# Performance work log

Measured on AMD Instinct MI355X. Metric: run time of the kernel, lower is better.

Reference implementation:

```python
import jax, jax.numpy as jnp
import numpy as np
import math

D, NH, NL, NP_ = 256, 8, 3, 4
BS, LQ = 32, 300
SHAPES = [(80, 80), (40, 40), (20, 20)]
LV = sum(h * w for h, w in SHAPES)  # 8400
DFF = 1024


def _offset_bias():
    # faithful to MSDeformableAttention._reset_parameters
    thetas = jnp.arange(NH, dtype=jnp.float32) * (2.0 * math.pi / NH)
    grid = jnp.stack([jnp.cos(thetas), jnp.sin(thetas)], -1)
    grid = grid / jnp.abs(grid).max(-1, keepdims=True)
    grid = jnp.tile(grid.reshape(NH, 1, 1, 2), (1, NL, NP_, 1))
    grid = grid * jnp.arange(1, NP_ + 1, dtype=jnp.float32).reshape(1, 1, -1, 1)
    return grid.reshape(-1)


def setup_inputs() -> dict:
    key = jax.random.key(0)
    ks = iter(jax.random.split(key, 64))
    rn = lambda shape, s=0.02: jax.random.normal(next(ks), shape, jnp.float32) * s
    z = lambda n: jnp.zeros((n,), jnp.float32)
    o = lambda n: jnp.ones((n,), jnp.float32)
    inp = {
        'tgt': jax.random.normal(next(ks), (BS, LQ, D), jnp.float32),
        'reference_points': jax.random.uniform(next(ks), (BS, LQ, NL, 2), jnp.float32),
        'memory': jax.random.normal(next(ks), (BS, LV, D), jnp.float32),
        'query_pos_embed': jax.random.normal(next(ks), (BS, LQ, D), jnp.float32),
        'memory_spatial_shapes': np.array(SHAPES, dtype=np.int64),
        'memory_level_start_index': np.array([0, 6400, 8000], dtype=np.int64),
        # self-attn
        'Wq': rn((D, D)), 'bq': z(D), 'Wk': rn((D, D)), 'bk': z(D),
        'Wv': rn((D, D)), 'bv': z(D), 'Wo': rn((D, D)), 'bo': z(D),
        'ln1_g': o(D), 'ln1_b': z(D),
        # deformable cross-attn
        'W_vproj': rn((D, D)), 'b_vproj': z(D),
        'W_off': rn((D, NH * NL * NP_ * 2), 0.001), 'b_off': _offset_bias(),
        'W_attn': rn((D, NH * NL * NP_)), 'b_attn': z(NH * NL * NP_),
        'W_out': rn((D, D)), 'b_out': z(D),
        'ln2_g': o(D), 'ln2_b': z(D),
        # FFN
        'W1': rn((D, DFF)), 'b1': z(DFF), 'W2': rn((DFF, D)), 'b2': z(D),
        'ln3_g': o(D), 'ln3_b': z(D),
    }
    return inp


def _ln(x, g, b):
    m = x.mean(-1, keepdims=True)
    v = ((x - m) ** 2).mean(-1, keepdims=True)
    return (x - m) / jnp.sqrt(v + 1e-5) * g + b


def _ms_deform(value, shapes, loc, aw):
    # value [bs,Lv,nh,c]; loc [bs,Lq,nh,NL,NP,2] in [0,1]; aw [bs,Lq,nh,NL,NP]
    bs, Lv, nh, c = value.shape
    Lq = loc.shape[1]
    npts = loc.shape[4]
    grids = 2.0 * loc - 1.0
    out = jnp.zeros((bs, nh, Lq, c), value.dtype)
    start = 0
    for lvl, (h, w) in enumerate(shapes):
        flat = value[:, start:start + h * w].transpose(0, 2, 1, 3)  # [bs,nh,hw,c]
        start += h * w
        g = grids[:, :, :, lvl].transpose(0, 2, 1, 3, 4).reshape(bs, nh, Lq * npts, 2)
        # align_corners=False pixel coords
        x = (g[..., 0] + 1.0) * (w / 2.0) - 0.5
        y = (g[..., 1] + 1.0) * (h / 2.0) - 0.5
        x0 = jnp.floor(x); y0 = jnp.floor(y)
        wx1 = x - x0; wy1 = y - y0
        samp = jnp.zeros((bs, nh, Lq * npts, c), value.dtype)
        for xi, yi, wgt in ((x0, y0, (1 - wx1) * (1 - wy1)),
                            (x0 + 1, y0, wx1 * (1 - wy1)),
                            (x0, y0 + 1, (1 - wx1) * wy1),
                            (x0 + 1, y0 + 1, wx1 * wy1)):
            valid = (xi >= 0) & (xi < w) & (yi >= 0) & (yi < h)
            idx = (jnp.clip(yi, 0, h - 1) * w + jnp.clip(xi, 0, w - 1)).astype(jnp.int32)
            idx = jnp.broadcast_to(idx[..., None], idx.shape + (c,))
            gv = jnp.take_along_axis(flat, idx, axis=2)  # [bs,nh,Lq*np,c]
            samp = samp + gv * (wgt * valid.astype(value.dtype))[..., None]
        samp = samp.reshape(bs, nh, Lq, npts, c)
        a = aw[:, :, :, lvl].transpose(0, 2, 1, 3)  # [bs,nh,Lq,np]
        out = out + (samp * a[..., None]).sum(3)
    return out.transpose(0, 2, 1, 3).reshape(bs, Lq, nh * c)


def reference(tgt, reference_points, memory, query_pos_embed,
              memory_spatial_shapes, memory_level_start_index,
              Wq, bq, Wk, bk, Wv, bv, Wo, bo, ln1_g, ln1_b,
              W_vproj, b_vproj, W_off, b_off, W_attn, b_attn, W_out, b_out,
              ln2_g, ln2_b, W1, b1, W2, b2, ln3_g, ln3_b):
    shapes = [(int(h), int(w)) for h, w in np.asarray(memory_spatial_shapes)]
    bs, Lq, d = tgt.shape
    hd = d // NH
    # --- self attention (dropout=eval identity, attn_mask=None) ---
    q = tgt + query_pos_embed
    qh = (q @ Wq + bq).reshape(bs, Lq, NH, hd)
    kh = (q @ Wk + bk).reshape(bs, Lq, NH, hd)
    vh = (tgt @ Wv + bv).reshape(bs, Lq, NH, hd)
    att = jax.nn.softmax(jnp.einsum('bqhd,bkhd->bhqk', qh, kh) / jnp.sqrt(jnp.float32(hd)), axis=-1)
    sa = jnp.einsum('bhqk,bkhd->bqhd', att, vh).reshape(bs, Lq, d) @ Wo + bo
    tgt = _ln(tgt + sa, ln1_g, ln1_b)
    # --- deformable cross attention ---
    qc = tgt + query_pos_embed
    value = (memory @ W_vproj + b_vproj).reshape(bs, -1, NH, hd)
    off = (qc @ W_off + b_off).reshape(bs, Lq, NH, NL, NP_, 2)
    aw = jax.nn.softmax((qc @ W_attn + b_attn).reshape(bs, Lq, NH, NL * NP_), axis=-1)
    aw = aw.reshape(bs, Lq, NH, NL, NP_)
    norm = jnp.array([[w, h] for h, w in shapes], jnp.float32)  # flip -> (w,h)
    loc = reference_points[:, :, None, :, None, :] + off / norm[None, None, None, :, None, :]
    ca = _ms_deform(value, shapes, loc, aw) @ W_out + b_out
    tgt = _ln(tgt + ca, ln2_g, ln2_b)
    # --- FFN ---
    h = jax.nn.relu(tgt @ W1 + b1) @ W2 + b2
    return _ln(tgt + h, ln3_g, ln3_b)
```

## Files before the change

### kernel.cpp

```cpp
#include <hip/hip_runtime.h>
#include <hip/hip_bf16.h>

#define D_      256
#define NH_     8
#define HD_     32
#define NL_     3
#define NP_4    4
#define BS_     32
#define LQ_     300
#define LV_     8400
#define DFF_    1024
#define NTOK    (BS_ * LQ_)
#define NVAL    (BS_ * LV_)

typedef __attribute__((ext_vector_type(8))) short bf16x8;
typedef __attribute__((ext_vector_type(4))) float f32x4;

__device__ inline unsigned short f2bf(float x) {
    union { float f; unsigned u; } v; v.f = x;
    unsigned r = v.u + 0x7FFFu + ((v.u >> 16) & 1u);
    return (unsigned short)(r >> 16);
}
__device__ inline float bf2f(unsigned short x) {
    union { unsigned u; float f; } v; v.u = ((unsigned)x) << 16;
    return v.f;
}

struct TrDesc { const float* W; unsigned short* Wt; int K; int N; };
struct TrPack { TrDesc d[10]; };

__global__ __launch_bounds__(256)
void tr_kernel(TrPack p) {
    TrDesc d = p.d[blockIdx.z];
    const int n0 = blockIdx.x * 32, k0 = blockIdx.y * 32;
    if (n0 >= d.N || k0 >= d.K) return;
    __shared__ float t[32][33];
    const int tx = threadIdx.x & 31, ty = threadIdx.x >> 5;
    #pragma unroll
    for (int i = 0; i < 4; ++i) {
        int k = k0 + ty + i * 8, n = n0 + tx;
        t[ty + i * 8][tx] = (k < d.K && n < d.N) ? d.W[(size_t)k * d.N + n] : 0.f;
    }
    __syncthreads();
    #pragma unroll
    for (int i = 0; i < 4; ++i) {
        int n = n0 + ty + i * 8, k = k0 + tx;
        if (n < d.N && k < d.K) d.Wt[(size_t)n * d.K + k] = f2bf(t[tx][ty + i * 8]);
    }
}

template <int ROWS, int COLS, int KK, int KC, int WR, int WC, int AMODE, int CMODE>
__global__ __launch_bounds__(256)
void gemm_os(const void* __restrict__ Ain, const float* __restrict__ A2,
             const unsigned short* __restrict__ Wt, const float* __restrict__ bias,
             void* __restrict__ Cout, int M, int N) {
    constexpr int LDK = KC + 8;
    constexpr int NC = KK / KC;
    constexpr int KS = KC / 32;
    constexpr int WROWS = ROWS / WR, WCOLS = COLS / WC;
    constexpr int RT = WROWS / 16, TC = WCOLS / 16;
    __shared__ unsigned short Alds[ROWS * LDK];
    __shared__ unsigned short Blds[COLS * LDK];

    const int tid = threadIdx.x, lane = tid & 63, w = tid >> 6;
    const int quad = lane >> 4, l16 = lane & 15;
    const int wr = w / WC, wc = w % WC;
    const int rowBase = blockIdx.y * ROWS;
    const int colBase = blockIdx.x * COLS;

    f32x4 acc[RT][TC];
    #pragma unroll
    for (int rt = 0; rt < RT; ++rt)
        #pragma unroll
        for (int j = 0; j < TC; ++j)
            #pragma unroll
            for (int r = 0; r < 4; ++r) acc[rt][j][r] = 0.f;

    for (int ch = 0; ch < NC; ++ch) {
        if (NC > 1) __syncthreads();
        {
            constexpr int CNT = ROWS * KC / 1024;
            if (AMODE == 2) {
                constexpr int CNT2 = ROWS * KC / 2048;
                #pragma unroll
                for (int i = 0; i < CNT2; ++i) {
                    int idx = i * 256 + tid;
                    int row = idx / (KC / 8), kofs = (idx % (KC / 8)) * 8;
                    int4 v = *(const int4*)((const unsigned short*)Ain +
                              (size_t)(rowBase + row) * KK + ch * KC + kofs);
                    *(int4*)&Alds[row * LDK + kofs] = v;
                }
            } else {
                #pragma unroll
                for (int i = 0; i < CNT; ++i) {
                    int idx = i * 256 + tid;
                    int row = idx / (KC / 4), kofs = (idx % (KC / 4)) * 4;
                    size_t g = (size_t)(rowBase + row) * KK + ch * KC + kofs;
                    float4 a = *(const float4*)((const float*)Ain + g);
                    if (AMODE == 1) {
                        float4 b = *(const float4*)(A2 + g);
                        a.x += b.x; a.y += b.y; a.z += b.z; a.w += b.w;
                    }
                    ushort4 s4;
                    s4.x = f2bf(a.x); s4.y = f2bf(a.y);
                    s4.z = f2bf(a.z); s4.w = f2bf(a.w);
                    *(ushort4*)&Alds[row * LDK + kofs] = s4;
                }
            }
        }
        {
            constexpr int CNT = COLS * KC / 2048;
            #pragma unroll
            for (int i = 0; i < CNT; ++i) {
                int idx = i * 256 + tid;
                int col = idx / (KC / 8), kofs = (idx % (KC / 8)) * 8;
                int4 v = *(const int4*)(Wt + (size_t)(colBase + col) * KK + ch * KC + kofs);
                *(int4*)&Blds[col * LDK + kofs] = v;
            }
        }
        __syncthreads();

        #pragma unroll
        for (int s = 0; s < KS; ++s) {
            bf16x8 af[RT], bf[TC];
            #pragma unroll
            for (int rt = 0; rt < RT; ++rt)
                af[rt] = *(const bf16x8*)&Alds[(wr * WROWS + rt * 16 + l16) * LDK + s * 32 + quad * 8];
            #pragma unroll
            for (int j = 0; j < TC; ++j)
                bf[j] = *(const bf16x8*)&Blds[(wc * WCOLS + j * 16 + l16) * LDK + s * 32 + quad * 8];
            #pragma unroll
            for (int rt = 0; rt < RT; ++rt)
                #pragma unroll
                for (int j = 0; j < TC; ++j)
                    acc[rt][j] = __builtin_amdgcn_mfma_f32_16x16x32_bf16(af[rt], bf[j], acc[rt][j], 0, 0, 0);
        }
    }

    #pragma unroll
    for (int rt = 0; rt < RT; ++rt) {
        #pragma unroll
        for (int j = 0; j < TC; ++j) {
            int col = colBase + wc * WCOLS + j * 16 + l16;
            float bb = bias[col];
            #pragma unroll
            for (int r = 0; r < 4; ++r) {
                int row = rowBase + wr * WROWS + rt * 16 + quad * 4 + r;
                float c = acc[rt][j][r] + bb;
                if (CMODE == 1 || CMODE == 3) c = fmaxf(c, 0.f);
                if (CMODE >= 2)
                    ((unsigned short*)Cout)[(size_t)row * N + col] = f2bf(c);
                else
                    ((float*)Cout)[(size_t)row * N + col] = c;
            }
        }
    }
}

#define PS_STRIDE 344
__global__ __launch_bounds__(256)
void attn_mfma(const unsigned short* __restrict__ qh,
               const unsigned short* __restrict__ kh,
               const unsigned short* __restrict__ vh,
               float* __restrict__ out) {
    __shared__ unsigned short Ps[4 * 16 * PS_STRIDE];
    __shared__ unsigned short Vs[32 * PS_STRIDE];
    const int tid = threadIdx.x;
    const int bh = blockIdx.x >> 1, half_ = blockIdx.x & 1;
    const int b = bh >> 3, h = bh & 7;
    const int w = tid >> 6, lane = tid & 63;
    const int quad = lane >> 4, l16 = lane & 15;

    for (int i = tid; i < 4 * 16 * PS_STRIDE / 2; i += 256) ((unsigned*)Ps)[i] = 0u;

    const size_t hbase = ((size_t)b * LQ_) * D_ + h * HD_;
    for (int it = 0; it < 10; ++it) {
        int chunk = tid + 256 * it;
        int key = chunk >> 3, cc = (chunk & 7) * 4;
        ushort4 v = make_ushort4(0, 0, 0, 0);
        if (key < LQ_) v = *(const ushort4*)(vh + hbase + (size_t)key * D_ + cc);
        Vs[(cc + 0) * PS_STRIDE + key] = v.x;
        Vs[(cc + 1) * PS_STRIDE + key] = v.y;
        Vs[(cc + 2) * PS_STRIDE + key] = v.z;
        Vs[(cc + 3) * PS_STRIDE + key] = v.w;
    }
    __syncthreads();

    const unsigned short* qb = qh + hbase;
    const unsigned short* kb = kh + hbase;
    const float scale = 0.17677669529663687f;

    for (int qt = 10 * half_ + w; qt < 10 * half_ + 10 && qt < 19; qt += 4) {
        int rowq = qt * 16 + l16; if (rowq > LQ_ - 1) rowq = LQ_ - 1;
        bf16x8 aq = *(const bf16x8*)(qb + (size_t)rowq * D_ + quad * 8);

        f32x4 S[19];
        #pragma unroll
        for (int kt = 0; kt < 19; ++kt) {
            int rowk = kt * 16 + l16; if (rowk > LQ_ - 1) rowk = LQ_ - 1;
            bf16x8 bk = *(const bf16x8*)(kb + (size_t)rowk * D_ + quad * 8);
            f32x4 z; z[0] = z[1] = z[2] = z[3] = 0.f;
            S[kt] = __builtin_amdgcn_mfma_f32_16x16x32_bf16(aq, bk, z, 0, 0, 0);
        }
        float mrow[4] = {-1e30f, -1e30f, -1e30f, -1e30f};
        #pragma unroll
        for (int kt = 0; kt < 19; ++kt) {
            bool masked = (kt == 18) && (l16 >= 12);
            #pragma unroll
            for (int r = 0; r < 4; ++r) {
                float s = masked ? -1e30f : S[kt][r] * scale;
                S[kt][r] = s;
                mrow[r] = fmaxf(mrow[r], s);
            }
        }
        #pragma unroll
        for (int r = 0; r < 4; ++r)
            #pragma unroll
            for (int off = 1; off < 16; off <<= 1)
                mrow[r] = fmaxf(mrow[r], __shfl_xor(mrow[r], off));
        float psum[4] = {0.f, 0.f, 0.f, 0.f};
        #pragma unroll
        for (int kt = 0; kt < 19; ++kt)
            #pragma unroll
            for (int r = 0; r < 4; ++r) {
                float p = __expf(S[kt][r] - mrow[r]);
                S[kt][r] = p;
                psum[r] += p;
            }
        #pragma unroll
        for (int r = 0; r < 4; ++r)
            #pragma unroll
            for (int off = 1; off < 16; off <<= 1)
                psum[r] += __shfl_xor(psum[r], off);
        float linv[4];
        #pragma unroll
        for (int r = 0; r < 4; ++r) linv[r] = 1.f / psum[r];

        unsigned short* pw = Ps + w * (16 * PS_STRIDE);
        #pragma unroll
        for (int kt = 0; kt < 19; ++kt)
            #pragma unroll
            for (int r = 0; r < 4; ++r)
                pw[(quad * 4 + r) * PS_STRIDE + kt * 16 + l16] = f2bf(S[kt][r]);

        f32x4 o0, o1;
        #pragma unroll
        for (int r = 0; r < 4; ++r) { o0[r] = 0.f; o1[r] = 0.f; }
        #pragma unroll
        for (int ks = 0; ks < 10; ++ks) {
            bf16x8 ap = *(const bf16x8*)(pw + l16 * PS_STRIDE + ks * 32 + quad * 8);
            bf16x8 b0 = *(const bf16x8*)(Vs + l16 * PS_STRIDE + ks * 32 + quad * 8);
            bf16x8 b1 = *(const bf16x8*)(Vs + (16 + l16) * PS_STRIDE + ks * 32 + quad * 8);
            o0 = __builtin_amdgcn_mfma_f32_16x16x32_bf16(ap, b0, o0, 0, 0, 0);
            o1 = __builtin_amdgcn_mfma_f32_16x16x32_bf16(ap, b1, o1, 0, 0, 0);
        }
        #pragma unroll
        for (int r = 0; r < 4; ++r) {
            int q = qt * 16 + quad * 4 + r;
            if (q < LQ_) {
                size_t ob = ((size_t)b * LQ_ + q) * D_ + h * HD_;
                out[ob + l16]      = o0[r] * linv[r];
                out[ob + 16 + l16] = o1[r] * linv[r];
            }
        }
    }
}

__global__ __launch_bounds__(256)
void ln_kernel(const float* __restrict__ x, const float* __restrict__ r,
               const float* __restrict__ g, const float* __restrict__ bta,
               float* __restrict__ out) {
    const int tok = blockIdx.x;
    const int t = threadIdx.x;
    float v = x[(size_t)tok * D_ + t] + r[(size_t)tok * D_ + t];

    float s = v;
    #pragma unroll
    for (int i = 1; i < 64; i <<= 1) s += __shfl_xor(s, i);
    __shared__ float red1[4];
    if ((t & 63) == 0) red1[t >> 6] = s;
    __syncthreads();
    float mean = (red1[0] + red1[1] + red1[2] + red1[3]) * (1.0f / D_);

    float d = v - mean;
    float s2 = d * d;
    #pragma unroll
    for (int i = 1; i < 64; i <<= 1) s2 += __shfl_xor(s2, i);
    __shared__ float red2[4];
    if ((t & 63) == 0) red2[t >> 6] = s2;
    __syncthreads();
    float var = (red2[0] + red2[1] + red2[2] + red2[3]) * (1.0f / D_);

    out[(size_t)tok * D_ + t] = d * rsqrtf(var + 1e-5f) * g[t] + bta[t];
}

__global__ __launch_bounds__(256)
void deform_kernel(const unsigned short* __restrict__ value,
                   const float* __restrict__ off,
                   const float* __restrict__ awl,
                   const float* __restrict__ ref,
                   float* __restrict__ out) {
    const int lvl_hw[3]    = {80, 40, 20};
    const int lvl_start[3] = {0, 6400, 8000};
    const int gid = blockIdx.x * 16 + (threadIdx.x >> 4);
    const int c2  = (threadIdx.x & 15) * 2;
    const int h   = gid & 7;
    const int bq  = gid >> 3;
    const int b   = bq / LQ_;

    float lg[12];
    const float* ap = awl + (size_t)bq * 96 + h * 12;
    float m = -1e30f;
    #pragma unroll
    for (int j = 0; j < 12; ++j) { lg[j] = ap[j]; m = fmaxf(m, lg[j]); }
    float s = 0.f;
    #pragma unroll
    for (int j = 0; j < 12; ++j) { lg[j] = __expf(lg[j] - m); s += lg[j]; }
    const float inv = 1.0f / s;

    const float* op = off + (size_t)bq * 192 + h * 24;
    const float* rp = ref + (size_t)bq * 6;

    float accx = 0.f, accy = 0.f;
    #pragma unroll
    for (int l = 0; l < NL_; ++l) {
        const int W = lvl_hw[l], H = lvl_hw[l];
        const float fw = (float)W, fh = (float)H;
        const float rx = rp[l * 2 + 0], ry = rp[l * 2 + 1];
        const unsigned short* vbase =
            value + ((size_t)b * LV_ + lvl_start[l]) * D_ + h * HD_ + c2;
        #pragma unroll
        for (int p = 0; p < NP_4; ++p) {
            float ox = op[(l * 4 + p) * 2 + 0], oy = op[(l * 4 + p) * 2 + 1];
            float x = (rx + ox / fw) * fw - 0.5f;
            float y = (ry + oy / fh) * fh - 0.5f;
            float x0f = floorf(x), y0f = floorf(y);
            float wx = x - x0f, wy = y - y0f;
            int x0 = (int)x0f, y0 = (int)y0f;
            float a = lg[l * 4 + p] * inv;
            const float cw[4] = {a * (1.f - wx) * (1.f - wy), a * wx * (1.f - wy),
                                 a * (1.f - wx) * wy,         a * wx * wy};
            const int cx[4] = {x0, x0 + 1, x0,     x0 + 1};
            const int cy[4] = {y0, y0,     y0 + 1, y0 + 1};
            #pragma unroll
            for (int cor = 0; cor < 4; ++cor) {
                int xi = cx[cor], yi = cy[cor];
                if (xi < 0 || xi >= W || yi < 0 || yi >= H) continue;
                unsigned v = *(const unsigned*)(vbase + (size_t)(yi * W + xi) * D_);
                accx += cw[cor] * bf2f((unsigned short)(v & 0xFFFFu));
                accy += cw[cor] * bf2f((unsigned short)(v >> 16));
            }
        }
    }
    float2 o2; o2.x = accx; o2.y = accy;
    *(float2*)(out + (size_t)bq * D_ + h * HD_ + c2) = o2;
}

extern "C" void kernel_launch(void* const* d_in, const int* in_sizes, int n_in,
                              void* d_out, int out_size, void* d_ws, size_t ws_size,
                              hipStream_t stream) {
    const float* tgt   = (const float*)d_in[0];
    const float* refpt = (const float*)d_in[1];
    const float* mem   = (const float*)d_in[2];
    const float* qpos  = (const float*)d_in[3];
    const float* Wq = (const float*)d_in[6],  *bq = (const float*)d_in[7];
    const float* Wk = (const float*)d_in[8],  *bk = (const float*)d_in[9];
    const float* Wv = (const float*)d_in[10], *bv = (const float*)d_in[11];
    const float* Wo = (const float*)d_in[12], *bo = (const float*)d_in[13];
    const float* ln1_g = (const float*)d_in[14], *ln1_b = (const float*)d_in[15];
    const float* W_vproj = (const float*)d_in[16], *b_vproj = (const float*)d_in[17];
    const float* W_off  = (const float*)d_in[18], *b_off  = (const float*)d_in[19];
    const float* W_attn = (const float*)d_in[20], *b_attn = (const float*)d_in[21];
    const float* W_out  = (const float*)d_in[22], *b_out  = (const float*)d_in[23];
    const float* ln2_g = (const float*)d_in[24], *ln2_b = (const float*)d_in[25];
    const float* W1 = (const float*)d_in[26], *b1 = (const float*)d_in[27];
    const float* W2 = (const float*)d_in[28], *b2 = (const float*)d_in[29];
    const float* ln3_g = (const float*)d_in[30], *ln3_b = (const float*)d_in[31];
    float* out = (float*)d_out;

    char* p = (char*)d_ws;
    const size_t TOKD = (size_t)NTOK * D_;
    float* buf_attn = (float*)p; p += TOKD * 4;
    float* buf_tmp  = (float*)p; p += TOKD * 4;
    float* buf_t1   = (float*)p; p += TOKD * 4;
    float* buf_t2   = (float*)p; p += TOKD * 4;
    unsigned short* buf_qh = (unsigned short*)p; p += TOKD * 2;
    unsigned short* buf_kh = (unsigned short*)p; p += TOKD * 2;
    unsigned short* buf_vh = (unsigned short*)p; p += TOKD * 2;
    float* buf_off  = (float*)p; p += (size_t)NTOK * 192 * 4;
    float* buf_awl  = (float*)p; p += (size_t)NTOK * 96 * 4;
    unsigned short* wt_q   = (unsigned short*)p; p += 65536 * 2;
    unsigned short* wt_k   = (unsigned short*)p; p += 65536 * 2;
    unsigned short* wt_v   = (unsigned short*)p; p += 65536 * 2;
    unsigned short* wt_o   = (unsigned short*)p; p += 65536 * 2;
    unsigned short* wt_vp  = (unsigned short*)p; p += 65536 * 2;
    unsigned short* wt_off = (unsigned short*)p; p += 49152 * 2;
    unsigned short* wt_awl = (unsigned short*)p; p += 24576 * 2;
    unsigned short* wt_out = (unsigned short*)p; p += 65536 * 2;
    unsigned short* wt_1   = (unsigned short*)p; p += (size_t)262144 * 2;
    unsigned short* wt_2   = (unsigned short*)p; p += (size_t)262144 * 2;
    unsigned short* buf_value = (unsigned short*)p;
    unsigned short* buf_ffnb  = (unsigned short*)p;

    TrPack pk;
    pk.d[0] = {Wq,      wt_q,   256, 256};
    pk.d[1] = {Wk,      wt_k,   256, 256};
    pk.d[2] = {Wv,      wt_v,   256, 256};
    pk.d[3] = {Wo,      wt_o,   256, 256};
    pk.d[4] = {W_vproj, wt_vp,  256, 256};
    pk.d[5] = {W_off,   wt_off, 256, 192};
    pk.d[6] = {W_attn,  wt_awl, 256, 96};
    pk.d[7] = {W_out,   wt_out, 256, 256};
    pk.d[8] = {W1,      wt_1,   256, 1024};
    pk.d[9] = {W2,      wt_2,   1024, 256};
    tr_kernel<<<dim3(32, 32, 10), 256, 0, stream>>>(pk);

    gemm_os<32, 128, 256, 128, 1, 4, 1, 2><<<dim3(2, NTOK / 32), 256, 0, stream>>>(
        tgt, qpos, wt_q, bq, buf_qh, NTOK, 256);
    gemm_os<32, 128, 256, 128, 1, 4, 1, 2><<<dim3(2, NTOK / 32), 256, 0, stream>>>(
        tgt, qpos, wt_k, bk, buf_kh, NTOK, 256);
    gemm_os<32, 128, 256, 128, 1, 4, 0, 2><<<dim3(2, NTOK / 32), 256, 0, stream>>>(
        tgt, nullptr, wt_v, bv, buf_vh, NTOK, 256);
    attn_mfma<<<BS_ * NH_ * 2, 256, 0, stream>>>(buf_qh, buf_kh, buf_vh, buf_attn);
    gemm_os<32, 128, 256, 128, 1, 4, 0, 0><<<dim3(2, NTOK / 32), 256, 0, stream>>>(
        buf_attn, nullptr, wt_o, bo, buf_tmp, NTOK, 256);
    ln_kernel<<<NTOK, 256, 0, stream>>>(tgt, buf_tmp, ln1_g, ln1_b, buf_t1);

    gemm_os<64, 128, 256, 128, 2, 2, 0, 2><<<dim3(2, NVAL / 64), 256, 0, stream>>>(
        mem, nullptr, wt_vp, b_vproj, buf_value, NVAL, 256);
    gemm_os<32, 192, 256, 128, 1, 4, 1, 0><<<dim3(1, NTOK / 32), 256, 0, stream>>>(
        buf_t1, qpos, wt_off, b_off, buf_off, NTOK, 192);
    gemm_os<32, 96, 256, 128, 2, 2, 1, 0><<<dim3(1, NTOK / 32), 256, 0, stream>>>(
        buf_t1, qpos, wt_awl, b_attn, buf_awl, NTOK, 96);
    deform_kernel<<<(BS_ * LQ_ * NH_) / 16, 256, 0, stream>>>(
        buf_value, buf_off, buf_awl, refpt, buf_attn);
    gemm_os<32, 128, 256, 128, 1, 4, 0, 0><<<dim3(2, NTOK / 32), 256, 0, stream>>>(
        buf_attn, nullptr, wt_out, b_out, buf_tmp, NTOK, 256);
    ln_kernel<<<NTOK, 256, 0, stream>>>(buf_t1, buf_tmp, ln2_g, ln2_b, buf_t2);

    gemm_os<32, 128, 256, 128, 1, 4, 0, 3><<<dim3(8, NTOK / 32), 256, 0, stream>>>(
        buf_t2, nullptr, wt_1, b1, buf_ffnb, NTOK, DFF_);
    gemm_os<32, 64, 1024, 256, 1, 4, 2, 0><<<dim3(4, NTOK / 32), 256, 0, stream>>>(
        buf_ffnb, nullptr, wt_2, b2, buf_tmp, NTOK, 256);
    ln_kernel<<<NTOK, 256, 0, stream>>>(buf_t2, buf_tmp, ln3_g, ln3_b, out);
}
```

Measured before the change: 700.3 us.

## Fuse residual LayerNorm into output GEMMs and batch QKV/offset GEMM launches

Adds a gemm_ln kernel in which each block computes a full 256-wide row tile, then applies bias, residual add and LayerNorm in the epilogue. This replaces three separate ln_kernel launches and the fp32 round trips through buf_tmp. The Q/K/V projections and the offset/attention-weight projections are each batched into one launch via a descriptor pack indexed by blockIdx.z. The attention and deform outputs are now written in bf16 to halve traffic into the next GEMM. Other changes: the value-projection chunk size is reduced, launch bounds are set to four blocks per CU, and LayerNorm variance is now computed as E[x²]−mean², which is slightly less numerically stable.

```diff
diff --git a/kernel.cpp b/kernel.cpp
--- a/kernel.cpp
+++ b/kernel.cpp
@@ -50,8 +50,8 @@
 }
 
 template <int ROWS, int COLS, int KK, int KC, int WR, int WC, int AMODE, int CMODE>
-__global__ __launch_bounds__(256)
-void gemm_os(const void* __restrict__ Ain, const float* __restrict__ A2,
+__global__ __launch_bounds__(256, 4)
+void gemm_os(const void* __restrict__ Ain,
              const unsigned short* __restrict__ Wt, const float* __restrict__ bias,
              void* __restrict__ Cout, int M, int N) {
     constexpr int LDK = KC + 8;
@@ -78,34 +78,28 @@
 
     for (int ch = 0; ch < NC; ++ch) {
         if (NC > 1) __syncthreads();
-        {
+        if (AMODE == 2) {
+            constexpr int CNT2 = ROWS * KC / 2048;
+            #pragma unroll
+            for (int i = 0; i < CNT2; ++i) {
+                int idx = i * 256 + tid;
+                int row = idx / (KC / 8), kofs = (idx % (KC / 8)) * 8;
+                int4 v = *(const int4*)((const unsigned short*)Ain +
+                          (size_t)(rowBase + row) * KK + ch * KC + kofs);
+                *(int4*)&Alds[row * LDK + kofs] = v;
+            }
+        } else {
             constexpr int CNT = ROWS * KC / 1024;
-            if (AMODE == 2) {
-                constexpr int CNT2 = ROWS * KC / 2048;
-                #pragma unroll
-                for (int i = 0; i < CNT2; ++i) {
-                    int idx = i * 256 + tid;
-                    int row = idx / (KC / 8), kofs = (idx % (KC / 8)) * 8;
-                    int4 v = *(const int4*)((const unsigned short*)Ain +
-                              (size_t)(rowBase + row) * KK + ch * KC + kofs);
-                    *(int4*)&Alds[row * LDK + kofs] = v;
-                }
-            } else {
-                #pragma unroll
-                for (int i = 0; i < CNT; ++i) {
-                    int idx = i * 256 + tid;
-                    int row = idx / (KC / 4), kofs = (idx % (KC / 4)) * 4;
-                    size_t g = (size_t)(rowBase + row) * KK + ch * KC + kofs;
-                    float4 a = *(const float4*)((const float*)Ain + g);
-                    if (AMODE == 1) {
-                        float4 b = *(const float4*)(A2 + g);
-                        a.x += b.x; a.y += b.y; a.z += b.z; a.w += b.w;
-                    }
-                    ushort4 s4;
-                    s4.x = f2bf(a.x); s4.y = f2bf(a.y);
-                    s4.z = f2bf(a.z); s4.w = f2bf(a.w);
-                    *(ushort4*)&Alds[row * LDK + kofs] = s4;
-                }
+            #pragma unroll
+            for (int i = 0; i < CNT; ++i) {
+                int idx = i * 256 + tid;
+                int row = idx / (KC / 4), kofs = (idx % (KC / 4)) * 4;
+                size_t gg = (size_t)(rowBase + row) * KK + ch * KC + kofs;
+                float4 a = *(const float4*)((const float*)Ain + gg);
+                ushort4 s4;
+                s4.x = f2bf(a.x); s4.y = f2bf(a.y);
+                s4.z = f2bf(a.z); s4.w = f2bf(a.w);
+                *(ushort4*)&Alds[row * LDK + kofs] = s4;
             }
         }
         {
@@ -122,18 +116,18 @@
 
         #pragma unroll
         for (int s = 0; s < KS; ++s) {
-            bf16x8 af[RT], bf[TC];
+            bf16x8 af[RT], bfr[TC];
             #pragma unroll
             for (int rt = 0; rt < RT; ++rt)
                 af[rt] = *(const bf16x8*)&Alds[(wr * WROWS + rt * 16 + l16) * LDK + s * 32 + quad * 8];
             #pragma unroll
             for (int j = 0; j < TC; ++j)
-                bf[j] = *(const bf16x8*)&Blds[(wc * WCOLS + j * 16 + l16) * LDK + s * 32 + quad * 8];
+                bfr[j] = *(const bf16x8*)&Blds[(wc * WCOLS + j * 16 + l16) * LDK + s * 32 + quad * 8];
             #pragma unroll
             for (int rt = 0; rt < RT; ++rt)
                 #pragma unroll
                 for (int j = 0; j < TC; ++j)
-                    acc[rt][j] = __builtin_amdgcn_mfma_f32_16x16x32_bf16(af[rt], bf[j], acc[rt][j], 0, 0, 0);
+                    acc[rt][j] = __builtin_amdgcn_mfma_f32_16x16x32_bf16(af[rt], bfr[j], acc[rt][j], 0, 0, 0);
         }
     }
 
@@ -147,11 +141,242 @@
             for (int r = 0; r < 4; ++r) {
                 int row = rowBase + wr * WROWS + rt * 16 + quad * 4 + r;
                 float c = acc[rt][j][r] + bb;
-                if (CMODE == 1 || CMODE == 3) c = fmaxf(c, 0.f);
+                if (CMODE == 3) c = fmaxf(c, 0.f);
                 if (CMODE >= 2)
                     ((unsigned short*)Cout)[(size_t)row * N + col] = f2bf(c);
                 else
                     ((float*)Cout)[(size_t)row * N + col] = c;
+            }
+        }
+    }
+}
+
+struct GDesc { const float* Ain; const float* A2; const unsigned short* Wt;
+               const float* bias; void* Cout; int N; };
+struct GPack3 { GDesc d[3]; };
+
+template <int ROWS, int COLS, int KK, int KC, int WR, int WC, int CMODE>
+__global__ __launch_bounds__(256, 4)
+void gemm_osb(GPack3 pk) {
+    constexpr int LDK = KC + 8;
+    constexpr int NC = KK / KC;
+    constexpr int KS = KC / 32;
+    constexpr int WROWS = ROWS / WR, WCOLS = COLS / WC;
+    constexpr int RT = WROWS / 16, TC = WCOLS / 16;
+    __shared__ unsigned short Alds[ROWS * LDK];
+    __shared__ unsigned short Blds[COLS * LDK];
+
+    GDesc g = pk.d[blockIdx.z];
+    const int colBase = blockIdx.x * COLS;
+    if (colBase >= g.N) return;
+    const int tid = threadIdx.x, lane = tid & 63, w = tid >> 6;
+    const int quad = lane >> 4, l16 = lane & 15;
+    const int wr = w / WC, wc = w % WC;
+    const int rowBase = blockIdx.y * ROWS;
+
+    f32x4 acc[RT][TC];
+    #pragma unroll
+    for (int rt = 0; rt < RT; ++rt)
+        #pragma unroll
+        for (int j = 0; j < TC; ++j)
+            #pragma unroll
+            for (int r = 0; r < 4; ++r) acc[rt][j][r] = 0.f;
+
+    for (int ch = 0; ch < NC; ++ch) {
+        if (NC > 1) __syncthreads();
+        {
+            constexpr int CNT = ROWS * KC / 1024;
+            #pragma unroll
+            for (int i = 0; i < CNT; ++i) {
+                int idx = i * 256 + tid;
+                int row = idx / (KC / 4), kofs = (idx % (KC / 4)) * 4;
+                size_t gg = (size_t)(rowBase + row) * KK + ch * KC + kofs;
+                float4 a = *(const float4*)(g.Ain + gg);
+                if (g.A2) {
+                    float4 b = *(const float4*)(g.A2 + gg);
+                    a.x += b.x; a.y += b.y; a.z += b.z; a.w += b.w;
+                }
+                ushort4 s4;
+                s4.x = f2bf(a.x); s4.y = f2bf(a.y);
+                s4.z = f2bf(a.z); s4.w = f2bf(a.w);
+                *(ushort4*)&Alds[row * LDK + kofs] = s4;
+            }
+        }
+        {
+            constexpr int CNT = COLS * KC / 2048;
+            #pragma unroll
+            for (int i = 0; i < CNT; ++i) {
+                int idx = i * 256 + tid;
+                int col = idx / (KC / 8), kofs = (idx % (KC / 8)) * 8;
+                int4 v = *(const int4*)(g.Wt + (size_t)(colBase + col) * KK + ch * KC + kofs);
+                *(int4*)&Blds[col * LDK + kofs] = v;
+            }
+        }
+        __syncthreads();
+
+        #pragma unroll
+        for (int s = 0; s < KS; ++s) {
+            bf16x8 af[RT], bfr[TC];
+            #pragma unroll
+            for (int rt = 0; rt < RT; ++rt)
+                af[rt] = *(const bf16x8*)&Alds[(wr * WROWS + rt * 16 + l16) * LDK + s * 32 + quad * 8];
+            #pragma unroll
+            for (int j = 0; j < TC; ++j)
+                bfr[j] = *(const bf16x8*)&Blds[(wc * WCOLS + j * 16 + l16) * LDK + s * 32 + quad * 8];
+            #pragma unroll
+            for (int rt = 0; rt < RT; ++rt)
+                #pragma unroll
+                for (int j = 0; j < TC; ++j)
+                    acc[rt][j] = __builtin_amdgcn_mfma_f32_16x16x32_bf16(af[rt], bfr[j], acc[rt][j], 0, 0, 0);
+        }
+    }
+
+    #pragma unroll
+    for (int rt = 0; rt < RT; ++rt) {
+        #pragma unroll
+        for (int j = 0; j < TC; ++j) {
+            int col = colBase + wc * WCOLS + j * 16 + l16;
+            float bb = g.bias[col];
+            #pragma unroll
+            for (int r = 0; r < 4; ++r) {
+                int row = rowBase + wr * WROWS + rt * 16 + quad * 4 + r;
+                float c = acc[rt][j][r] + bb;
+                if (CMODE >= 2)
+                    ((unsigned short*)g.Cout)[(size_t)row * g.N + col] = f2bf(c);
+                else
+                    ((float*)g.Cout)[(size_t)row * g.N + col] = c;
+            }
+        }
+    }
+}
+
+template <int KK, int KC>
+__global__ __launch_bounds__(256)
+void gemm_ln(const unsigned short* __restrict__ Ain,
+             const unsigned short* __restrict__ Wt, const float* __restrict__ bias,
+             const float* __restrict__ xres, const float* __restrict__ lng,
+             const float* __restrict__ lnb, float* __restrict__ Cout) {
+    constexpr int ROWS = 32, COLS = 256;
+    constexpr int LDK = KC + 8;
+    constexpr int NC = KK / KC;
+    constexpr int KS = KC / 32;
+    constexpr int RT = 2, TC = 4;
+    __shared__ unsigned short Alds[ROWS * LDK];
+    __shared__ unsigned short Blds[COLS * LDK];
+    __shared__ float redS[4][32];
+    __shared__ float redQ[4][32];
+
+    const int tid = threadIdx.x, lane = tid & 63, w = tid >> 6;
+    const int quad = lane >> 4, l16 = lane & 15;
+    const int wc = w;
+    const int rowBase = blockIdx.x * ROWS;
+
+    f32x4 acc[RT][TC];
+    #pragma unroll
+    for (int rt = 0; rt < RT; ++rt)
+        #pragma unroll
+        for (int j = 0; j < TC; ++j)
+            #pragma unroll
+            for (int r = 0; r < 4; ++r) acc[rt][j][r] = 0.f;
+
+    for (int ch = 0; ch < NC; ++ch) {
+        if (NC > 1) __syncthreads();
+        {
+            constexpr int CNT2 = ROWS * KC / 2048;
+            #pragma unroll
+            for (int i = 0; i < CNT2; ++i) {
+                int idx = i * 256 + tid;
+                int row = idx / (KC / 8), kofs = (idx % (KC / 8)) * 8;
+                int4 v = *(const int4*)(Ain + (size_t)(rowBase + row) * KK + ch * KC + kofs);
+                *(int4*)&Alds[row * LDK + kofs] = v;
+            }
+        }
+        {
+            constexpr int CNT = COLS * KC / 2048;
+            #pragma unroll
+            for (int i = 0; i < CNT; ++i) {
+                int idx = i * 256 + tid;
+                int col = idx / (KC / 8), kofs = (idx % (KC / 8)) * 8;
+                int4 v = *(const int4*)(Wt + (size_t)col * KK + ch * KC + kofs);
+                *(int4*)&Blds[col * LDK + kofs] = v;
+            }
+        }
+        __syncthreads();
+
+        #pragma unroll
+        for (int s = 0; s < KS; ++s) {
+            bf16x8 af[RT], bfr[TC];
+            #pragma unroll
+            for (int rt = 0; rt < RT; ++rt)
+                af[rt] = *(const bf16x8*)&Alds[(rt * 16 + l16) * LDK + s * 32 + quad * 8];
+            #pragma unroll
+            for (int j = 0; j < TC; ++j)
+                bfr[j] = *(const bf16x8*)&Blds[(wc * 64 + j * 16 + l16) * LDK + s * 32 + quad * 8];
+            #pragma unroll
+            for (int rt = 0; rt < RT; ++rt)
+                #pragma unroll
+                for (int j = 0; j < TC; ++j)
+                    acc[rt][j] = __builtin_amdgcn_mfma_f32_16x16x32_bf16(af[rt], bfr[j], acc[rt][j], 0, 0, 0);
+        }
+    }
+
+    float p[RT][4], q[RT][4];
+    #pragma unroll
+    for (int rt = 0; rt < RT; ++rt)
+        #pragma unroll
+        for (int r = 0; r < 4; ++r) { p[rt][r] = 0.f; q[rt][r] = 0.f; }
+
+    #pragma unroll
+    for (int rt = 0; rt < RT; ++rt) {
+        #pragma unroll
+        for (int j = 0; j < TC; ++j) {
+            int col = wc * 64 + j * 16 + l16;
+            float bb = bias[col];
+            #pragma unroll
+            for (int r = 0; r < 4; ++r) {
+                int row = rowBase + rt * 16 + quad * 4 + r;
+                float v = acc[rt][j][r] + bb + xres[(size_t)row * 256 + col];
+                acc[rt][j][r] = v;
+                p[rt][r] += v;
+                q[rt][r] += v * v;
+            }
+        }
+    }
+    #pragma unroll
+    for (int rt = 0; rt < RT; ++rt)
+        #pragma unroll
+        for (int r = 0; r < 4; ++r)
+            #pragma unroll
+            for (int off = 1; off < 16; off <<= 1) {
+                p[rt][r] += __shfl_xor(p[rt][r], off);
+                q[rt][r] += __shfl_xor(q[rt][r], off);
+            }
+    if (l16 == 0) {
+        #pragma unroll
+        for (int rt = 0; rt < RT; ++rt)
+            #pragma unroll
+            for (int r = 0; r < 4; ++r) {
+                redS[w][rt * 16 + quad * 4 + r] = p[rt][r];
+                redQ[w][rt * 16 + quad * 4 + r] = q[rt][r];
+            }
+    }
+    __syncthreads();
+    #pragma unroll
+    for (int rt = 0; rt < RT; ++rt) {
+        #pragma unroll
+        for (int r = 0; r < 4; ++r) {
+            int ridx = rt * 16 + quad * 4 + r;
+            float s  = redS[0][ridx] + redS[1][ridx] + redS[2][ridx] + redS[3][ridx];
+            float ss = redQ[0][ridx] + redQ[1][ridx] + redQ[2][ridx] + redQ[3][ridx];
+            float mean = s * (1.0f / 256.0f);
+            float var  = ss * (1.0f / 256.0f) - mean * mean;
+            float inv  = rsqrtf(var + 1e-5f);
+            int row = rowBase + ridx;
+            #pragma unroll
+            for (int j = 0; j < TC; ++j) {
+                int col = wc * 64 + j * 16 + l16;
+                Cout[(size_t)row * 256 + col] =
+                    (acc[rt][j][r] - mean) * inv * lng[col] + lnb[col];
             }
         }
     }
@@ -162,7 +387,7 @@
 void attn_mfma(const unsigned short* __restrict__ qh,
                const unsigned short* __restrict__ kh,
                const unsigned short* __restrict__ vh,
-               float* __restrict__ out) {
+               unsigned short* __restrict__ out) {
     __shared__ unsigned short Ps[4 * 16 * PS_STRIDE];
     __shared__ unsigned short Vs[32 * PS_STRIDE];
     const int tid = threadIdx.x;
@@ -223,9 +448,9 @@
         for (int kt = 0; kt < 19; ++kt)
             #pragma unroll
             for (int r = 0; r < 4; ++r) {
-                float p = __expf(S[kt][r] - mrow[r]);
-                S[kt][r] = p;
-                psum[r] += p;
+                float pcur = __expf(S[kt][r] - mrow[r]);
+                S[kt][r] = pcur;
+                psum[r] += pcur;
             }
         #pragma unroll
         for (int r = 0; r < 4; ++r)
@@ -259,39 +484,11 @@
             int q = qt * 16 + quad * 4 + r;
             if (q < LQ_) {
                 size_t ob = ((size_t)b * LQ_ + q) * D_ + h * HD_;
-                out[ob + l16]      = o0[r] * linv[r];
-                out[ob + 16 + l16] = o1[r] * linv[r];
-            }
-        }
-    }
-}
-
-__global__ __launch_bounds__(256)
-void ln_kernel(const float* __restrict__ x, const float* __restrict__ r,
-               const float* __restrict__ g, const float* __restrict__ bta,
-               float* __restrict__ out) {
-    const int tok = blockIdx.x;
-    const int t = threadIdx.x;
-    float v = x[(size_t)tok * D_ + t] + r[(size_t)tok * D_ + t];
-
-    float s = v;
-    #pragma unroll
-    for (int i = 1; i < 64; i <<= 1) s += __shfl_xor(s, i);
-    __shared__ float red1[4];
-    if ((t & 63) == 0) red1[t >> 6] = s;
-    __syncthreads();
-    float mean = (red1[0] + red1[1] + red1[2] + red1[3]) * (1.0f / D_);
-
-    float d = v - mean;
-    float s2 = d * d;
-    #pragma unroll
-    for (int i = 1; i < 64; i <<= 1) s2 += __shfl_xor(s2, i);
-    __shared__ float red2[4];
-    if ((t & 63) == 0) red2[t >> 6] = s2;
-    __syncthreads();
-    float var = (red2[0] + red2[1] + red2[2] + red2[3]) * (1.0f / D_);
-
-    out[(size_t)tok * D_ + t] = d * rsqrtf(var + 1e-5f) * g[t] + bta[t];
+                out[ob + l16]      = f2bf(o0[r] * linv[r]);
+                out[ob + 16 + l16] = f2bf(o1[r] * linv[r]);
+            }
+        }
+    }
 }
 
 __global__ __launch_bounds__(256)
@@ -299,7 +496,7 @@
                    const float* __restrict__ off,
                    const float* __restrict__ awl,
                    const float* __restrict__ ref,
-                   float* __restrict__ out) {
+                   unsigned short* __restrict__ out) {
     const int lvl_hw[3]    = {80, 40, 20};
     const int lvl_start[3] = {0, 6400, 8000};
     const int gid = blockIdx.x * 16 + (threadIdx.x >> 4);
@@ -352,8 +549,8 @@
             }
         }
     }
-    float2 o2; o2.x = accx; o2.y = accy;
-    *(float2*)(out + (size_t)bq * D_ + h * HD_ + c2) = o2;
+    unsigned pack = (unsigned)f2bf(accx) | ((unsigned)f2bf(accy) << 16);
+    *(unsigned*)(out + (size_t)bq * D_ + h * HD_ + c2) = pack;
 }
 
 extern "C" void kernel_launch(void* const* d_in, const int* in_sizes, int n_in,
@@ -415,32 +612,30 @@
     pk.d[9] = {W2,      wt_2,   1024, 256};
     tr_kernel<<<dim3(32, 32, 10), 256, 0, stream>>>(pk);
 
-    gemm_os<32, 128, 256, 128, 1, 4, 1, 2><<<dim3(2, NTOK / 32), 256, 0, stream>>>(
-        tgt, qpos, wt_q, bq, buf_qh, NTOK, 256);
-    gemm_os<32, 128, 256, 128, 1, 4, 1, 2><<<dim3(2, NTOK / 32), 256, 0, stream>>>(
-        tgt, qpos, wt_k, bk, buf_kh, NTOK, 256);
-    gemm_os<32, 128, 256, 128, 1, 4, 0, 2><<<dim3(2, NTOK / 32), 256, 0, stream>>>(
-        tgt, nullptr, wt_v, bv, buf_vh, NTOK, 256);
-    attn_mfma<<<BS_ * NH_ * 2, 256, 0, stream>>>(buf_qh, buf_kh, buf_vh, buf_attn);
-    gemm_os<32, 128, 256, 128, 1, 4, 0, 0><<<dim3(2, NTOK / 32), 256, 0, stream>>>(
-        buf_attn, nullptr, wt_o, bo, buf_tmp, NTOK, 256);
-    ln_kernel<<<NTOK, 256, 0, stream>>>(tgt, buf_tmp, ln1_g, ln1_b, buf_t1);
-
-    gemm_os<64, 128, 256, 128, 2, 2, 0, 2><<<dim3(2, NVAL / 64), 256, 0, stream>>>(
-        mem, nullptr, wt_vp, b_vproj, buf_value, NVAL, 256);
-    gemm_os<32, 192, 256, 128, 1, 4, 1, 0><<<dim3(1, NTOK / 32), 256, 0, stream>>>(
-        buf_t1, qpos, wt_off, b_off, buf_off, NTOK, 192);
-    gemm_os<32, 96, 256, 128, 2, 2, 1, 0><<<dim3(1, NTOK / 32), 256, 0, stream>>>(
-        buf_t1, qpos, wt_awl, b_attn, buf_awl, NTOK, 96);
+    GPack3 qkv;
+    qkv.d[0] = {tgt, qpos,    wt_q, bq, buf_qh, 256};
+    qkv.d[1] = {tgt, qpos,    wt_k, bk, buf_kh, 256};
+    qkv.d[2] = {tgt, nullptr, wt_v, bv, buf_vh, 256};
+    gemm_osb<32, 128, 256, 128, 1, 4, 2><<<dim3(2, NTOK / 32, 3), 256, 0, stream>>>(qkv);
+    attn_mfma<<<BS_ * NH_ * 2, 256, 0, stream>>>(buf_qh, buf_kh, buf_vh,
+                                                 (unsigned short*)buf_attn);
+    gemm_ln<256, 128><<<NTOK / 32, 256, 0, stream>>>(
+        (const unsigned short*)buf_attn, wt_o, bo, tgt, ln1_g, ln1_b, buf_t1);
+
+    gemm_os<64, 128, 256, 64, 2, 2, 0, 2><<<dim3(2, NVAL / 64), 256, 0, stream>>>(
+        mem, wt_vp, b_vproj, buf_value, NVAL, 256);
+    GPack3 oa;
+    oa.d[0] = {buf_t1, qpos, wt_off, b_off,  buf_off, 192};
+    oa.d[1] = {buf_t1, qpos, wt_awl, b_attn, buf_awl, 96};
+    oa.d[2] = oa.d[1];
+    gemm_osb<32, 96, 256, 128, 2, 2, 0><<<dim3(2, NTOK / 32, 2), 256, 0, stream>>>(oa);
     deform_kernel<<<(BS_ * LQ_ * NH_) / 16, 256, 0, stream>>>(
-        buf_value, buf_off, buf_awl, refpt, buf_attn);
-    gemm_os<32, 128, 256, 128, 1, 4, 0, 0><<<dim3(2, NTOK / 32), 256, 0, stream>>>(
-        buf_attn, nullptr, wt_out, b_out, buf_tmp, NTOK, 256);
-    ln_kernel<<<NTOK, 256, 0, stream>>>(buf_t1, buf_tmp, ln2_g, ln2_b, buf_t2);
+        buf_value, buf_off, buf_awl, refpt, (unsigned short*)buf_attn);
+    gemm_ln<256, 128><<<NTOK / 32, 256, 0, stream>>>(
+        (const unsigned short*)buf_attn, wt_out, b_out, buf_t1, ln2_g, ln2_b, buf_t2);
 
     gemm_os<32, 128, 256, 128, 1, 4, 0, 3><<<dim3(8, NTOK / 32), 256, 0, stream>>>(
-        buf_t2, nullptr, wt_1, b1, buf_ffnb, NTOK, DFF_);
-    gemm_os<32, 64, 1024, 256, 1, 4, 2, 0><<<dim3(4, NTOK / 32), 256, 0, stream>>>(
-        buf_ffnb, nullptr, wt_2, b2, buf_tmp, NTOK, 256);
-    ln_kernel<<<NTOK, 256, 0, stream>>>(buf_t2, buf_tmp, ln3_g, ln3_b, out);
-}
+        buf_t2, wt_1, b1, buf_ffnb, NTOK, DFF_);
+    gemm_ln<1024, 128><<<NTOK / 32, 256, 0, stream>>>(
+        buf_ffnb, wt_2, b2, buf_t2, ln3_g, ln3_b, out);
+}
```

New measurement: 750.6 us. 1.07x slower.
